# Kernel tuning notes

Hardware: AMD Instinct MI355X
Metric: run time of the kernel (lower is better)

The kernel has to match this reference:

```python
import jax, jax.numpy as jnp
import numpy as np

D_MODEL = 1024
NUM_HEADS = 16
D_K = D_MODEL // NUM_HEADS


def setup_inputs() -> dict:
    key = jax.random.key(0)
    ks = jax.random.split(key, 12)
    B, S = 4, 2048
    scale = 1.0 / np.sqrt(D_MODEL)
    inp = {
        "query": jax.random.normal(ks[0], (B, S, D_MODEL), dtype=jnp.float32),
        "key": jax.random.normal(ks[1], (B, S, D_MODEL), dtype=jnp.float32),
        "value": jax.random.normal(ks[2], (B, S, D_MODEL), dtype=jnp.float32),
        "Wq": jax.random.normal(ks[3], (D_MODEL, D_MODEL), dtype=jnp.float32) * scale,
        "bq": jnp.zeros((D_MODEL,), dtype=jnp.float32),
        "Wk": jax.random.normal(ks[4], (D_MODEL, D_MODEL), dtype=jnp.float32) * scale,
        "bk": jnp.zeros((D_MODEL,), dtype=jnp.float32),
        "Wv": jax.random.normal(ks[5], (D_MODEL, D_MODEL), dtype=jnp.float32) * scale,
        "bv": jnp.zeros((D_MODEL,), dtype=jnp.float32),
        "Wo": jax.random.normal(ks[6], (D_MODEL, D_MODEL), dtype=jnp.float32) * scale,
        "bo": jnp.zeros((D_MODEL,), dtype=jnp.float32),
    }
    return inp


def reference(query, key, value, Wq, bq, Wk, bk, Wv, bv, Wo, bo):
    B, S, _ = query.shape
    # project and split heads: [B, S, D] -> [B, H, S, d_k]
    def split_heads(x):
        return x.reshape(B, -1, NUM_HEADS, D_K).transpose(0, 2, 1, 3)

    q = split_heads(query @ Wq + bq)
    k = split_heads(key @ Wk + bk)
    v = split_heads(value @ Wv + bv)

    # scores: [B, H, Sq, Sk]
    scores = jnp.einsum("bhqd,bhkd->bhqk", q, k) / jnp.sqrt(jnp.float32(D_K))
    p_attn = jax.nn.softmax(scores, axis=-1)
    out = jnp.einsum("bhqk,bhkd->bhqd", p_attn, v)  # [B, H, Sq, d_k]

    out = out.transpose(0, 2, 1, 3).reshape(B, -1, NUM_HEADS * D_K)
    return out @ Wo + bo
```

## Files before the change

### kernel.cpp

```cpp
#include <hip/hip_runtime.h>
#include <hip/hip_bf16.h>

#define D_MODEL 1024
#define SEQ     2048
#define BATCH   4
#define HEADS   16
#define DKK     64
#define MTOT    (BATCH*SEQ)

typedef __attribute__((ext_vector_type(8)))  __bf16 bf16x8;
typedef __attribute__((ext_vector_type(4)))  float  f32x4;
typedef __attribute__((ext_vector_type(16))) float  f32x16;
typedef unsigned short u16;
typedef __attribute__((address_space(1))) const unsigned GU;
typedef __attribute__((address_space(3))) unsigned LU;

__device__ __forceinline__ u16 f2bf(float f) {
    unsigned u = __builtin_bit_cast(unsigned, f);
    u += 0x7FFFu + ((u >> 16) & 1u);
    return (u16)(u >> 16);
}

__device__ __forceinline__ unsigned pk2(float a, float b) {
    u16 x = __builtin_bit_cast(u16, (__bf16)a);
    u16 y = __builtin_bit_cast(u16, (__bf16)b);
    return (unsigned)x | ((unsigned)y << 16);
}

__device__ __forceinline__ float exp2_hw(float x) {
    return __builtin_amdgcn_exp2f(x);
}

__global__ void f2b3_kernel(const float* __restrict__ q, const float* __restrict__ k,
                            const float* __restrict__ v,
                            u16* __restrict__ oq, u16* __restrict__ ok, u16* __restrict__ ov,
                            int n4) {
    const float* in = (blockIdx.y == 0) ? q : (blockIdx.y == 1) ? k : v;
    u16* out = (blockIdx.y == 0) ? oq : (blockIdx.y == 1) ? ok : ov;
    int stride = gridDim.x * blockDim.x;
    for (int i = blockIdx.x * blockDim.x + threadIdx.x; i < n4; i += stride) {
        float4 x = reinterpret_cast<const float4*>(in)[i];
        ushort4 o;
        o.x = f2bf(x.x); o.y = f2bf(x.y); o.z = f2bf(x.z); o.w = f2bf(x.w);
        reinterpret_cast<ushort4*>(out)[i] = o;
    }
}

__global__ void wtrans4_kernel(const float* __restrict__ W0, const float* __restrict__ W1,
                               const float* __restrict__ W2, const float* __restrict__ W3,
                               u16* __restrict__ T0, u16* __restrict__ T1,
                               u16* __restrict__ T2, u16* __restrict__ T3) {
    const float* W = (blockIdx.z == 0) ? W0 : (blockIdx.z == 1) ? W1 : (blockIdx.z == 2) ? W2 : W3;
    u16* Wt = (blockIdx.z == 0) ? T0 : (blockIdx.z == 1) ? T1 : (blockIdx.z == 2) ? T2 : T3;
    __shared__ float t[32][33];
    int bx = blockIdx.x * 32, by = blockIdx.y * 32;
    int x = threadIdx.x, y0 = threadIdx.y;
    for (int y = y0; y < 32; y += 8)
        t[y][x] = W[(size_t)(by + y) * D_MODEL + bx + x];
    __syncthreads();
    for (int y = y0; y < 32; y += 8)
        Wt[(size_t)(bx + y) * D_MODEL + by + x] = f2bf(t[x][y]);
}

__global__ void vtrans_kernel(const u16* __restrict__ Vhp, u16* __restrict__ VT) {
    __shared__ u16 t[64][72];
    int bh = blockIdx.y, s0 = blockIdx.x * 64;
    int tid = threadIdx.x;
#pragma unroll
    for (int c = tid; c < 512; c += 256) {
        int r = c >> 3, ch = c & 7;
        *reinterpret_cast<bf16x8*>(&t[r][ch * 8]) =
            *reinterpret_cast<const bf16x8*>(Vhp + ((size_t)bh * SEQ + s0 + r) * DKK + ch * 8);
    }
    __syncthreads();
#pragma unroll
    for (int c = tid; c < 512; c += 256) {
        int d = c >> 3, ch = c & 7;
        union { bf16x8 v; u16 e[8]; } u;
#pragma unroll
        for (int j = 0; j < 8; j++) u.e[j] = t[ch * 8 + j][d];
        *reinterpret_cast<bf16x8*>(VT + ((size_t)bh * DKK + d) * SEQ + s0 + ch * 8) = u.v;
    }
}

__global__ __launch_bounds__(256) void gemm_pipe(
        const u16* __restrict__ A0, const u16* __restrict__ A1, const u16* __restrict__ A2,
        const u16* __restrict__ B0, const u16* __restrict__ B1, const u16* __restrict__ B2,
        const float* __restrict__ bi0, const float* __restrict__ bi1, const float* __restrict__ bi2,
        u16* __restrict__ o0, u16* __restrict__ o1, u16* __restrict__ o2,
        float* __restrict__ outf, int mode, float scale0)
{
    __shared__ __align__(16) char smem[3][16384];

    const int z = blockIdx.z;
    const u16* A  = (z == 0) ? A0 : (z == 1) ? A1 : A2;
    const u16* Bt = (z == 0) ? B0 : (z == 1) ? B1 : B2;
    const float* bias = (z == 0) ? bi0 : (z == 1) ? bi1 : bi2;
    u16* outb = (z == 0) ? o0 : (z == 1) ? o1 : o2;
    const float scale = (z == 0) ? scale0 : 1.0f;

    const int tid = threadIdx.x;
    const int m0 = blockIdx.y * 128, n0 = blockIdx.x * 128;
    const int w = tid >> 6, lane = tid & 63;
    const int l15 = lane & 15, lg = lane >> 4;
    const int wr = w >> 1, wc = w & 1;

    f32x4 acc[4][4];
#pragma unroll
    for (int i = 0; i < 4; i++)
#pragma unroll
        for (int j = 0; j < 4; j++) acc[i][j] = (f32x4){0.f, 0.f, 0.f, 0.f};

    auto stage = [&](int buf, int k0) {
        u16* Al = (u16*)(smem[buf]);
        u16* Bl = (u16*)(smem[buf] + 8192);
#pragma unroll
        for (int c = tid; c < 512; c += 256) {
            int row = c >> 2, ch = c & 3;
            __builtin_amdgcn_global_load_lds(
                (GU*)(A + (size_t)(m0 + row) * D_MODEL + k0 + ch * 8),
                (LU*)(Al + c * 8), 16, 0, 0);
            __builtin_amdgcn_global_load_lds(
                (GU*)(Bt + (size_t)(n0 + row) * D_MODEL + k0 + ch * 8),
                (LU*)(Bl + c * 8), 16, 0, 0);
        }
    };

    auto compute = [&](int buf) {
        const u16* Al = (const u16*)(smem[buf]);
        const u16* Bl = (const u16*)(smem[buf] + 8192);
        bf16x8 af[4], bfr[4];
#pragma unroll
        for (int m = 0; m < 4; m++)
            af[m] = *reinterpret_cast<const bf16x8*>(&Al[(wr * 64 + m * 16 + l15) * 32 + lg * 8]);
#pragma unroll
        for (int n = 0; n < 4; n++)
            bfr[n] = *reinterpret_cast<const bf16x8*>(&Bl[(wc * 64 + n * 16 + l15) * 32 + lg * 8]);
        __builtin_amdgcn_s_setprio(1);
#pragma unroll
        for (int m = 0; m < 4; m++)
#pragma unroll
            for (int n = 0; n < 4; n++)
                acc[m][n] = __builtin_amdgcn_mfma_f32_16x16x32_bf16(af[m], bfr[n], acc[m][n], 0, 0, 0);
        __builtin_amdgcn_s_setprio(0);
    };

    stage(0, 0);
    stage(1, 32);
    for (int t = 0; t < 32; ++t) {
        if (t < 31) asm volatile("s_waitcnt vmcnt(4)" ::: "memory");
        else        asm volatile("s_waitcnt vmcnt(0)" ::: "memory");
        __builtin_amdgcn_s_barrier();
        __builtin_amdgcn_sched_barrier(0);
        if (t + 2 < 32) stage((t + 2) % 3, (t + 2) * 32);
        compute(t % 3);
    }

#pragma unroll
    for (int n = 0; n < 4; n++) {
        int col = n0 + wc * 64 + n * 16 + l15;
        float bv = bias[col];
#pragma unroll
        for (int m = 0; m < 4; m++) {
            int rowb = m0 + wr * 64 + m * 16 + lg * 4;
#pragma unroll
            for (int r = 0; r < 4; r++) {
                int row = rowb + r;
                float v = (acc[m][n][r] + bv) * scale;
                if (mode == 0) {
                    int b = row >> 11, s = row & (SEQ - 1);
                    int h = col >> 6,  d = col & 63;
                    outb[(((size_t)b * HEADS + h) * SEQ + s) * DKK + d] = f2bf(v);
                } else {
                    outf[(size_t)row * D_MODEL + col] = v;
                }
            }
        }
    }
}

__global__ __launch_bounds__(512, 2) void attn8_kernel(
        const u16* __restrict__ Qh, const u16* __restrict__ Kh,
        const u16* __restrict__ VT, u16* __restrict__ ctx)
{
    __shared__ __align__(16) char smem[3][16384];

    const int i = blockIdx.x;
    const int xcd = i & 7, j = i >> 3;
    const int bh = xcd + 8 * (j & 7);
    const int bx = j >> 3;
    const int b = bh >> 4, h = bh & 15;
    const int tid = threadIdx.x, w = tid >> 6, lane = tid & 63;
    const int l31 = lane & 31, hi = lane >> 5;
    const int q0 = bx * 256 + w * 32;

    const u16* Qp = Qh + ((size_t)bh * SEQ + q0 + l31) * DKK + 8 * hi;
    bf16x8 qf[4];
#pragma unroll
    for (int c = 0; c < 4; c++)
        qf[c] = *reinterpret_cast<const bf16x8*>(Qp + 16 * c);

    const char* Kbyte = (const char*)(Kh + (size_t)bh * SEQ * DKK);
    const char* Vbyte = (const char*)(VT + (size_t)bh * DKK * SEQ);

    f32x16 zv;
#pragma unroll
    for (int z = 0; z < 16; z++) zv[z] = 0.f;
    f32x16 oacc0 = zv, oacc1 = zv;
    float lsum = 0.f;

    const int kr = tid >> 3, kc = tid & 7;
    const int ksw = (kc ^ (kr & 7)) * 16;

    auto stage = [&](int buf, int kt) {
        char* Kb = smem[buf];
        char* Vb = smem[buf] + 8192;
        __builtin_amdgcn_global_load_lds((GU*)(Kbyte + (size_t)(kt + kr) * 128 + ksw),
                                         (LU*)(Kb + tid * 16), 16, 0, 0);
        __builtin_amdgcn_global_load_lds((GU*)(Vbyte + (size_t)kr * (SEQ * 2) + kt * 2 + ksw),
                                         (LU*)(Vb + tid * 16), 16, 0, 0);
    };

    auto compute = [&](int buf) {
        const char* Kb = smem[buf];
        const char* Vb = smem[buf] + 8192;
        const int xr = (l31 & 7);

        bf16x8 kf[8];
#pragma unroll
        for (int c = 0; c < 4; c++) {
            int sl = ((2 * c + hi) ^ xr) * 16;
            kf[c]     = *reinterpret_cast<const bf16x8*>(Kb + l31 * 128 + sl);
            kf[c + 4] = *reinterpret_cast<const bf16x8*>(Kb + (l31 + 32) * 128 + sl);
        }

        __builtin_amdgcn_s_setprio(1);
        f32x16 s0 = __builtin_amdgcn_mfma_f32_32x32x16_bf16(kf[0], qf[0], zv, 0, 0, 0);
        f32x16 s1 = __builtin_amdgcn_mfma_f32_32x32x16_bf16(kf[4], qf[0], zv, 0, 0, 0);
#pragma unroll
        for (int c = 1; c < 4; c++) {
            s0 = __builtin_amdgcn_mfma_f32_32x32x16_bf16(kf[c],     qf[c], s0, 0, 0, 0);
            s1 = __builtin_amdgcn_mfma_f32_32x32x16_bf16(kf[c + 4], qf[c], s1, 0, 0, 0);
        }
        __builtin_amdgcn_s_setprio(0);

#pragma unroll
        for (int i2 = 0; i2 < 16; i2++) { s0[i2] = exp2_hw(s0[i2]); s1[i2] = exp2_hw(s1[i2]); }
        float a0 = (s0[0] + s0[1]) + (s0[2] + s0[3]);
        float a1 = (s0[4] + s0[5]) + (s0[6] + s0[7]);
        float a2 = (s0[8] + s0[9]) + (s0[10] + s0[11]);
        float a3 = (s0[12] + s0[13]) + (s0[14] + s0[15]);
        float b0 = (s1[0] + s1[1]) + (s1[2] + s1[3]);
        float b1 = (s1[4] + s1[5]) + (s1[6] + s1[7]);
        float b2 = (s1[8] + s1[9]) + (s1[10] + s1[11]);
        float b3 = (s1[12] + s1[13]) + (s1[14] + s1[15]);
        lsum += ((a0 + a1) + (a2 + a3)) + ((b0 + b1) + (b2 + b3));

#pragma unroll
        for (int t = 0; t < 4; t++) {
            const int o = 8 * (t & 1);
            float p0, p1, p2, p3, p4, p5, p6, p7;
            if (t < 2) {
                p0 = s0[o+0]; p1 = s0[o+1]; p2 = s0[o+2]; p3 = s0[o+3];
                p4 = s0[o+4]; p5 = s0[o+5]; p6 = s0[o+6]; p7 = s0[o+7];
            } else {
                p0 = s1[o+0]; p1 = s1[o+1]; p2 = s1[o+2]; p3 = s1[o+3];
                p4 = s1[o+4]; p5 = s1[o+5]; p6 = s1[o+6]; p7 = s1[o+7];
            }
            unsigned pkA = pk2(p0, p1);
            unsigned pkB = pk2(p2, p3);
            unsigned pkC = pk2(p4, p5);
            unsigned pkD = pk2(p6, p7);
            unsigned y1 = hi ? pkA : pkC;
            unsigned y2 = hi ? pkB : pkD;
            unsigned sy1 = __shfl_xor(y1, 32, 64);
            unsigned sy2 = __shfl_xor(y2, 32, 64);
            union { unsigned u[4]; bf16x8 v; } pu;
            pu.u[0] = hi ? sy1 : pkA;
            pu.u[1] = hi ? sy2 : pkB;
            pu.u[2] = hi ? pkC : sy1;
            pu.u[3] = hi ? pkD : sy2;
            bf16x8 pf = pu.v;

            int sl = ((2 * t + hi) ^ xr) * 16;
            bf16x8 vf0 = *reinterpret_cast<const bf16x8*>(Vb + l31 * 128 + sl);
            bf16x8 vf1 = *reinterpret_cast<const bf16x8*>(Vb + (l31 + 32) * 128 + sl);
            __builtin_amdgcn_s_setprio(1);
            oacc0 = __builtin_amdgcn_mfma_f32_32x32x16_bf16(vf0, pf, oacc0, 0, 0, 0);
            oacc1 = __builtin_amdgcn_mfma_f32_32x32x16_bf16(vf1, pf, oacc1, 0, 0, 0);
            __builtin_amdgcn_s_setprio(0);
        }
    };

    stage(0, 0);
    stage(1, 64);
    for (int t = 0; t < 32; ++t) {
        if (t < 31) asm volatile("s_waitcnt vmcnt(2)" ::: "memory");
        else        asm volatile("s_waitcnt vmcnt(0)" ::: "memory");
        __builtin_amdgcn_s_barrier();
        __builtin_amdgcn_sched_barrier(0);
        if (t + 2 < 32) stage((t + 2) % 3, (t + 2) * 64);
        compute(t % 3);
    }
    __syncthreads();

    lsum += __shfl_xor(lsum, 32, 64);
    float inv = 1.0f / lsum;

    typedef u16 OtArr[32][72];
    OtArr* Ot = reinterpret_cast<OtArr*>(smem);
#pragma unroll
    for (int r = 0; r < 16; r++) {
        int d0 = (r & 3) + 8 * (r >> 2) + 4 * hi;
        Ot[w][l31][d0]      = f2bf(oacc0[r] * inv);
        Ot[w][l31][d0 + 32] = f2bf(oacc1[r] * inv);
    }
    __syncthreads();
#pragma unroll
    for (int it = 0; it < 4; it++) {
        int r = (lane >> 3) + 8 * it, ch = lane & 7;
        bf16x8 v = *reinterpret_cast<const bf16x8*>(&Ot[w][r][ch * 8]);
        *reinterpret_cast<bf16x8*>(ctx + ((size_t)b * SEQ + q0 + r) * D_MODEL + h * DKK + ch * 8) = v;
    }
}

extern "C" void kernel_launch(void* const* d_in, const int* in_sizes, int n_in,
                              void* d_out, int out_size, void* d_ws, size_t ws_size,
                              hipStream_t stream)
{
    (void)in_sizes; (void)n_in; (void)out_size; (void)ws_size;

    const float* query = (const float*)d_in[0];
    const float* key   = (const float*)d_in[1];
    const float* value = (const float*)d_in[2];
    const float* Wq    = (const float*)d_in[3];
    const float* bq    = (const float*)d_in[4];
    const float* Wk    = (const float*)d_in[5];
    const float* bk    = (const float*)d_in[6];
    const float* Wv    = (const float*)d_in[7];
    const float* bv    = (const float*)d_in[8];
    const float* Wo    = (const float*)d_in[9];
    const float* bo    = (const float*)d_in[10];
    float* out = (float*)d_out;

    char* ws = (char*)d_ws;
    const size_t MB = 1024ull * 1024ull;
    u16* Xq  = (u16*)(ws);
    u16* Xk  = (u16*)(ws + 16 * MB);
    u16* Xv  = (u16*)(ws + 32 * MB);
    u16* Wtq = (u16*)(ws + 48 * MB);
    u16* Wtk = (u16*)(ws + 50 * MB);
    u16* Wtv = (u16*)(ws + 52 * MB);
    u16* Wto = (u16*)(ws + 54 * MB);
    u16* Qhp = (u16*)(ws + 56 * MB);
    u16* Khp = (u16*)(ws + 72 * MB);
    u16* Vhp = (u16*)(ws + 88 * MB);
    u16* ctx = (u16*)(ws + 104 * MB);
    u16* VT  = Xq;

    int nX4 = MTOT * D_MODEL / 4;
    f2b3_kernel<<<dim3(1024, 3), 256, 0, stream>>>(query, key, value, Xq, Xk, Xv, nX4);

    dim3 wg(32, 32, 4), wb(32, 8);
    wtrans4_kernel<<<wg, wb, 0, stream>>>(Wq, Wk, Wv, Wo, Wtq, Wtk, Wtv, Wto);

    dim3 g3(D_MODEL / 128, MTOT / 128, 3);
    gemm_pipe<<<g3, 256, 0, stream>>>(Xq, Xk, Xv, Wtq, Wtk, Wtv, bq, bk, bv,
                                      Qhp, Khp, Vhp, nullptr, 0, 0.125f * 1.44269504f);

    dim3 vg(SEQ / 64, BATCH * HEADS);
    vtrans_kernel<<<vg, 256, 0, stream>>>(Vhp, VT);

    attn8_kernel<<<512, 512, 0, stream>>>(Qhp, Khp, VT, ctx);

    dim3 g1(D_MODEL / 128, MTOT / 128, 1);
    gemm_pipe<<<g1, 256, 0, stream>>>(ctx, ctx, ctx, Wto, Wto, Wto, bo, bo, bo,
                                      nullptr, nullptr, nullptr, out, 1, 1.0f);
}
```

Before: 234.3 us.

## Fuse V transpose into QKV GEMM epilogue and permute K rows to drop P shuffles

```diff
diff --git a/kernel.cpp b/kernel.cpp
--- a/kernel.cpp
+++ b/kernel.cpp
@@ -62,27 +62,6 @@
         Wt[(size_t)(bx + y) * D_MODEL + by + x] = f2bf(t[x][y]);
 }
 
-__global__ void vtrans_kernel(const u16* __restrict__ Vhp, u16* __restrict__ VT) {
-    __shared__ u16 t[64][72];
-    int bh = blockIdx.y, s0 = blockIdx.x * 64;
-    int tid = threadIdx.x;
-#pragma unroll
-    for (int c = tid; c < 512; c += 256) {
-        int r = c >> 3, ch = c & 7;
-        *reinterpret_cast<bf16x8*>(&t[r][ch * 8]) =
-            *reinterpret_cast<const bf16x8*>(Vhp + ((size_t)bh * SEQ + s0 + r) * DKK + ch * 8);
-    }
-    __syncthreads();
-#pragma unroll
-    for (int c = tid; c < 512; c += 256) {
-        int d = c >> 3, ch = c & 7;
-        union { bf16x8 v; u16 e[8]; } u;
-#pragma unroll
-        for (int j = 0; j < 8; j++) u.e[j] = t[ch * 8 + j][d];
-        *reinterpret_cast<bf16x8*>(VT + ((size_t)bh * DKK + d) * SEQ + s0 + ch * 8) = u.v;
-    }
-}
-
 __global__ __launch_bounds__(256) void gemm_pipe(
         const u16* __restrict__ A0, const u16* __restrict__ A1, const u16* __restrict__ A2,
         const u16* __restrict__ B0, const u16* __restrict__ B1, const u16* __restrict__ B2,
@@ -160,26 +139,36 @@
     for (int n = 0; n < 4; n++) {
         int col = n0 + wc * 64 + n * 16 + l15;
         float bv = bias[col];
+        int h = col >> 6, d = col & 63;
 #pragma unroll
         for (int m = 0; m < 4; m++) {
             int rowb = m0 + wr * 64 + m * 16 + lg * 4;
-#pragma unroll
-            for (int r = 0; r < 4; r++) {
-                int row = rowb + r;
-                float v = (acc[m][n][r] + bv) * scale;
-                if (mode == 0) {
-                    int b = row >> 11, s = row & (SEQ - 1);
-                    int h = col >> 6,  d = col & 63;
-                    outb[(((size_t)b * HEADS + h) * SEQ + s) * DKK + d] = f2bf(v);
+            if (mode == 0) {
+                int b = rowb >> 11, s0r = rowb & (SEQ - 1);
+                if (z == 2) {
+                    ushort4 pk;
+                    pk.x = f2bf(acc[m][n][0] + bv);
+                    pk.y = f2bf(acc[m][n][1] + bv);
+                    pk.z = f2bf(acc[m][n][2] + bv);
+                    pk.w = f2bf(acc[m][n][3] + bv);
+                    *reinterpret_cast<ushort4*>(
+                        &outb[(((size_t)b * HEADS + h) * DKK + d) * SEQ + s0r]) = pk;
                 } else {
-                    outf[(size_t)row * D_MODEL + col] = v;
+#pragma unroll
+                    for (int r = 0; r < 4; r++)
+                        outb[(((size_t)b * HEADS + h) * SEQ + s0r + r) * DKK + d] =
+                            f2bf((acc[m][n][r] + bv) * scale);
                 }
+            } else {
+#pragma unroll
+                for (int r = 0; r < 4; r++)
+                    outf[(size_t)(rowb + r) * D_MODEL + col] = acc[m][n][r] + bv;
             }
         }
     }
 }
 
-__global__ __launch_bounds__(512, 2) void attn8_kernel(
+__global__ __launch_bounds__(512, 2) void attn9_kernel(
         const u16* __restrict__ Qh, const u16* __restrict__ Kh,
         const u16* __restrict__ VT, u16* __restrict__ ctx)
 {
@@ -211,11 +200,12 @@
 
     const int kr = tid >> 3, kc = tid & 7;
     const int ksw = (kc ^ (kr & 7)) * 16;
+    const int krp = (kr & 51) | ((kr & 4) << 1) | ((kr & 8) >> 1);
 
     auto stage = [&](int buf, int kt) {
         char* Kb = smem[buf];
         char* Vb = smem[buf] + 8192;
-        __builtin_amdgcn_global_load_lds((GU*)(Kbyte + (size_t)(kt + kr) * 128 + ksw),
+        __builtin_amdgcn_global_load_lds((GU*)(Kbyte + (size_t)(kt + krp) * 128 + ksw),
                                          (LU*)(Kb + tid * 16), 16, 0, 0);
         __builtin_amdgcn_global_load_lds((GU*)(Vbyte + (size_t)kr * (SEQ * 2) + kt * 2 + ksw),
                                          (LU*)(Vb + tid * 16), 16, 0, 0);
@@ -259,27 +249,18 @@
 #pragma unroll
         for (int t = 0; t < 4; t++) {
             const int o = 8 * (t & 1);
-            float p0, p1, p2, p3, p4, p5, p6, p7;
+            union { unsigned u[4]; bf16x8 v; } pu;
             if (t < 2) {
-                p0 = s0[o+0]; p1 = s0[o+1]; p2 = s0[o+2]; p3 = s0[o+3];
-                p4 = s0[o+4]; p5 = s0[o+5]; p6 = s0[o+6]; p7 = s0[o+7];
+                pu.u[0] = pk2(s0[o+0], s0[o+1]);
+                pu.u[1] = pk2(s0[o+2], s0[o+3]);
+                pu.u[2] = pk2(s0[o+4], s0[o+5]);
+                pu.u[3] = pk2(s0[o+6], s0[o+7]);
             } else {
-                p0 = s1[o+0]; p1 = s1[o+1]; p2 = s1[o+2]; p3 = s1[o+3];
-                p4 = s1[o+4]; p5 = s1[o+5]; p6 = s1[o+6]; p7 = s1[o+7];
+                pu.u[0] = pk2(s1[o+0], s1[o+1]);
+                pu.u[1] = pk2(s1[o+2], s1[o+3]);
+                pu.u[2] = pk2(s1[o+4], s1[o+5]);
+                pu.u[3] = pk2(s1[o+6], s1[o+7]);
             }
-            unsigned pkA = pk2(p0, p1);
-            unsigned pkB = pk2(p2, p3);
-            unsigned pkC = pk2(p4, p5);
-            unsigned pkD = pk2(p6, p7);
-            unsigned y1 = hi ? pkA : pkC;
-            unsigned y2 = hi ? pkB : pkD;
-            unsigned sy1 = __shfl_xor(y1, 32, 64);
-            unsigned sy2 = __shfl_xor(y2, 32, 64);
-            union { unsigned u[4]; bf16x8 v; } pu;
-            pu.u[0] = hi ? sy1 : pkA;
-            pu.u[1] = hi ? sy2 : pkB;
-            pu.u[2] = hi ? pkC : sy1;
-            pu.u[3] = hi ? pkD : sy2;
             bf16x8 pf = pu.v;
 
             int sl = ((2 * t + hi) ^ xr) * 16;
@@ -354,9 +335,8 @@
     u16* Wto = (u16*)(ws + 54 * MB);
     u16* Qhp = (u16*)(ws + 56 * MB);
     u16* Khp = (u16*)(ws + 72 * MB);
-    u16* Vhp = (u16*)(ws + 88 * MB);
+    u16* VT  = (u16*)(ws + 88 * MB);
     u16* ctx = (u16*)(ws + 104 * MB);
-    u16* VT  = Xq;
 
     int nX4 = MTOT * D_MODEL / 4;
     f2b3_kernel<<<dim3(1024, 3), 256, 0, stream>>>(query, key, value, Xq, Xk, Xv, nX4);
@@ -366,12 +346,9 @@
 
     dim3 g3(D_MODEL / 128, MTOT / 128, 3);
     gemm_pipe<<<g3, 256, 0, stream>>>(Xq, Xk, Xv, Wtq, Wtk, Wtv, bq, bk, bv,
-                                      Qhp, Khp, Vhp, nullptr, 0, 0.125f * 1.44269504f);
-
-    dim3 vg(SEQ / 64, BATCH * HEADS);
-    vtrans_kernel<<<vg, 256, 0, stream>>>(Vhp, VT);
-
-    attn8_kernel<<<512, 512, 0, stream>>>(Qhp, Khp, VT, ctx);
+                                      Qhp, Khp, VT, nullptr, 0, 0.125f * 1.44269504f);
+
+    attn9_kernel<<<512, 512, 0, stream>>>(Qhp, Khp, VT, ctx);
 
     dim3 g1(D_MODEL / 128, MTOT / 128, 1);
     gemm_pipe<<<g1, 256, 0, stream>>>(ctx, ctx, ctx, Wto, Wto, Wto, bo, bo, bo,
```

Measured after the change: 221.6 us. -5.4%, faster.
